# Optimization experiments

Hardware: AMD Instinct MI355X
Metric: run time of the kernel (lower is better)

The kernel has to match this reference:

```python
import jax, jax.numpy as jnp
import numpy as np

E = 8        # moe_num_experts
TOPK = 2     # moe_topk
H = 1024     # hidden_size
I = 1024     # intermediate_size
ISH = I * 2  # shared experts intermediate (intermediate_size * moe_num_shared_experts)
B, S = 2, 1024


def setup_inputs() -> dict:
    key = jax.random.key(0)
    ks = jax.random.split(key, 7)
    s = 0.02
    return {
        "hidden_states": jax.random.normal(ks[0], (B, S, H), jnp.float32),
        "w_router": jax.random.normal(ks[1], (H, E), jnp.float32) * s,
        "fc1_w": jax.random.normal(ks[2], (E, H, 2 * I), jnp.float32) * s,
        "fc2_w": jax.random.normal(ks[3], (E, I, H), jnp.float32) * s,
        "gate_w": jax.random.normal(ks[4], (H, ISH), jnp.float32) * s,
        "up_w": jax.random.normal(ks[5], (H, ISH), jnp.float32) * s,
        "down_w": jax.random.normal(ks[6], (ISH, H), jnp.float32) * s,
    }


def reference(hidden_states, w_router, fc1_w, fc2_w, gate_w, up_w, down_w):
    orig_shape = hidden_states.shape
    x = hidden_states.reshape(-1, orig_shape[-1])  # [N, H]

    # --- router: top-k + softmax over the top-k logits ---
    logits = x @ w_router                               # [N, E]
    top_logits, top_idx = jax.lax.top_k(logits, TOPK)   # [N, K]
    scores = jax.nn.softmax(top_logits, axis=-1)        # [N, K]

    # --- permute tokens so same-expert tokens are contiguous ---
    flat_idx = top_idx.reshape(-1)                      # [N*K]
    sorted_idx = jnp.argsort(flat_idx)                  # [N*K]
    permuted = x[sorted_idx // TOPK]                    # [N*K, H]
    eid = flat_idx[sorted_idx]                          # expert id per permuted slot

    # --- grouped expert SwiGLU MLP (masked per-expert GEMMs; masked rows
    #     contribute exactly zero since silu(0)*0 = 0 and 0 @ W = 0) ---
    out_perm = jnp.zeros((permuted.shape[0], orig_shape[-1]), x.dtype)
    for e in range(E):
        m = (eid == e).astype(x.dtype)[:, None]         # [N*K, 1]
        h1 = (permuted * m) @ fc1_w[e]                  # [N*K, 2I]
        proj, gate = jnp.split(h1, 2, axis=-1)
        out_perm = out_perm + (jax.nn.silu(proj) * gate) @ fc2_w[e]

    # --- unpermute and combine with router scores ---
    unperm = jnp.zeros_like(out_perm).at[sorted_idx].set(out_perm)  # [N*K, H]
    moe_out = (unperm.reshape(-1, TOPK, orig_shape[-1]) * scores[:, :, None]).sum(axis=1)
    moe_out = moe_out.reshape(orig_shape)

    # --- shared experts (LlamaMLP, SwiGLU) ---
    shared = (jax.nn.silu(hidden_states @ gate_w) * (hidden_states @ up_w)) @ down_w
    return moe_out + shared
```

## Files before the change

### kernel.cpp

```cpp
#include <hip/hip_runtime.h>
#include <cstdint>


#define E_ 8
#define H_ 1024
#define I_ 1024
#define ISH_ 2048
#define NTOK 2048

typedef unsigned short u16;
using bf16x8 = __attribute__((ext_vector_type(8))) __bf16;
using f32x4  = __attribute__((ext_vector_type(4))) float;

__device__ __forceinline__ u16 f2bf(float f) {
  union { float f; unsigned u; } v; v.f = f;
  unsigned r = v.u + 0x7fffu + ((v.u >> 16) & 1u);
  return (u16)(r >> 16);
}
__device__ __forceinline__ float bf2f(u16 u) {
  union { unsigned u; float f; } v; v.u = ((unsigned)u) << 16; return v.f;
}
__device__ __forceinline__ unsigned pk2(float lo, float hi) {
  return ((unsigned)f2bf(hi) << 16) | (unsigned)f2bf(lo);
}

typedef __attribute__((address_space(1))) const void glb_v;
typedef __attribute__((address_space(3))) void lds_v;
__device__ __forceinline__ void gl16(const void* g, void* l) {
  __builtin_amdgcn_global_load_lds((glb_v*)g, (lds_v*)l, 16, 0, 0);
}

__device__ __forceinline__ void router_body(const float* __restrict__ x,
                                            const float* __restrict__ wr,
                                            float* __restrict__ scores,
                                            int* __restrict__ cnt,
                                            int* __restrict__ list, int tk) {
  int lane = threadIdx.x & 63;
  const float* xr = x + (size_t)tk * H_;
  float acc[E_];
#pragma unroll
  for (int e = 0; e < E_; ++e) acc[e] = 0.f;
  int h0 = lane * 16;
#pragma unroll 4
  for (int i = 0; i < 16; ++i) {
    float xv = xr[h0 + i];
    const float* w = wr + (size_t)(h0 + i) * E_;
#pragma unroll
    for (int e = 0; e < E_; ++e) acc[e] = fmaf(xv, w[e], acc[e]);
  }
#pragma unroll
  for (int off = 32; off > 0; off >>= 1) {
#pragma unroll
    for (int e = 0; e < E_; ++e) acc[e] += __shfl_xor(acc[e], off, 64);
  }
  if (lane == 0) {
    int e0 = 0; float m0 = acc[0];
#pragma unroll
    for (int e = 1; e < E_; ++e) if (acc[e] > m0) { m0 = acc[e]; e0 = e; }
    int e1 = -1; float m1 = -1e30f;
#pragma unroll
    for (int e = 0; e < E_; ++e) if (e != e0 && acc[e] > m1) { m1 = acc[e]; e1 = e; }
    float s0 = 1.f / (1.f + __expf(m1 - m0));
    scores[tk * 2 + 0] = s0;
    scores[tk * 2 + 1] = 1.f - s0;
    int p0 = atomicAdd(&cnt[e0], 1); list[e0 * NTOK + p0] = tk * 2;
    int p1 = atomicAdd(&cnt[e1], 1); list[e1 * NTOK + p1] = tk * 2 + 1;
  }
}

__device__ __forceinline__ void wtrans(const float* __restrict__ src,
                                       u16* __restrict__ dst, int K, int N,
                                       int k0, int n0, void* smem) {
  unsigned* lt = (unsigned*)smem;
  int t = threadIdx.x;
  int c = t & 31, kb = t >> 5;
  const float* sp = src + (size_t)(k0 + kb * 8) * N + n0 + (c << 2);
  float v[8][4];
#pragma unroll
  for (int j2 = 0; j2 < 8; ++j2) {
    float4 f = *(const float4*)(sp + (size_t)j2 * N);
    v[j2][0] = f.x; v[j2][1] = f.y; v[j2][2] = f.z; v[j2][3] = f.w;
  }
#pragma unroll
  for (int j = 0; j < 4; ++j) {
    int nl = (c << 2) + j;
    uint4 o = make_uint4(pk2(v[0][j], v[1][j]), pk2(v[2][j], v[3][j]),
                         pk2(v[4][j], v[5][j]), pk2(v[6][j], v[7][j]));
    *(uint4*)&lt[nl * 32 + ((kb ^ (c & 7)) << 2)] = o;
  }
  __syncthreads();
#pragma unroll
  for (int it = 0; it < 4; ++it) {
    int lin = it * 256 + t;
    int nl = lin >> 3, kq = lin & 7;
    uint4 o = *(const uint4*)&lt[nl * 32 + ((kq ^ ((nl >> 2) & 7)) << 2)];
    *(uint4*)(dst + (size_t)(n0 + nl) * K + k0 + kq * 8) = o;
  }
}


__global__ __launch_bounds__(256) void prep_k(
    const float* __restrict__ x, const float* __restrict__ wr,
    float* __restrict__ scores, int* __restrict__ cnt, int* __restrict__ list,
    u16* __restrict__ xb,
    const float* __restrict__ fc1, const float* __restrict__ gw,
    const float* __restrict__ uw,
    u16* __restrict__ fc1T, u16* __restrict__ gwT, u16* __restrict__ uwT) {
  __shared__ __align__(16) char psm[16384];
  int bid = blockIdx.x, t = threadIdx.x;
  if (bid < 512) {
    router_body(x, wr, scores, cnt, list, bid * 4 + (t >> 6));
    return;
  }
  if (bid < 1024) {
    const float4* srcx = (const float4*)x;
    ushort4* dstx = (ushort4*)xb;
    int base = (bid - 512) * 1024 + t;
#pragma unroll
    for (int it = 0; it < 4; ++it) {
      float4 v = srcx[base + it * 256];
      ushort4 o;
      o.x = f2bf(v.x); o.y = f2bf(v.y); o.z = f2bf(v.z); o.w = f2bf(v.w);
      dstx[base + it * 256] = o;
    }
    return;
  }
  if (bid < 3072) {
    int b = bid - 1024;
    int e = b >> 8, q = b & 255;
    wtrans(fc1 + ((size_t)e << 21), fc1T + ((size_t)e << 21), 1024, 2048,
           (q & 15) * 64, (q >> 4) * 128, psm);
  } else if (bid < 3328) {
    int q = bid - 3072;
    wtrans(gw, gwT, 1024, 2048, (q & 15) * 64, (q >> 4) * 128, psm);
  } else {
    int q = bid - 3328;
    wtrans(uw, uwT, 1024, 2048, (q & 15) * 64, (q >> 4) * 128, psm);
  }
}

__global__ __launch_bounds__(256, 2) void swiglu_f_k(
    const u16* __restrict__ xb, const int* __restrict__ cnt,
    const int* __restrict__ list, const u16* __restrict__ fc1T,
    const u16* __restrict__ gwT, const u16* __restrict__ uwT,
    u16* __restrict__ act, u16* __restrict__ tmp,
    const float* __restrict__ fc2, const float* __restrict__ dw,
    u16* __restrict__ fc2T, u16* __restrict__ dwT) {
  __shared__ __align__(16) char smem[24576];
  if (blockIdx.x & 1) {
    int r = blockIdx.x >> 1;
    if (r < 1024) {
      int e = r >> 7, q = r & 127;
      wtrans(fc2 + ((size_t)e << 20), fc2T + ((size_t)e << 20), 1024, 1024,
             (q & 15) * 64, (q >> 4) * 128, smem);
    } else {
      int q = r - 1024;
      wtrans(dw, dwT, 2048, 1024, (q & 31) * 64, (q >> 5) * 128, smem);
    }
    return;
  }
  u16 (*As)[32]  = (u16(*)[32])smem;
  u16 (*B1s)[32] = (u16(*)[32])(smem + 8192);
  u16 (*B2s)[32] = (u16(*)[32])(smem + 16384);

  int bid = blockIdx.x >> 1;
  int m0, n0, Me, obase = 0, ldo;
  const u16 *B1, *B2;
  const int* rowmap = nullptr;
  u16* Out;
  if (bid < 256) {
    int mb = bid >> 4, nb = bid & 15;
    m0 = mb * 128; n0 = nb * 128; Me = NTOK;
    B1 = gwT + (size_t)n0 * 1024; B2 = uwT + (size_t)n0 * 1024;
    Out = tmp; ldo = ISH_;
  } else {
    int b2 = bid - 256; int e = b2 >> 7, r = b2 & 127, mb = r >> 3, nb = r & 7;
    Me = cnt[e]; m0 = mb * 128;
    if (m0 >= Me) return;
    n0 = nb * 128;
    rowmap = list + e * NTOK;
    const u16* fe = fc1T + ((size_t)e << 21);
    B1 = fe + (size_t)n0 * 1024;
    B2 = fe + (size_t)(1024 + n0) * 1024;
    int off = 0;
    for (int q = 0; q < e; ++q) off += cnt[q];
    obase = off;
    Out = act; ldo = I_;
  }
  int t = threadIdx.x, wid = t >> 6, lane = t & 63;
  int wm = wid & 1, wn = wid >> 1, lr = lane & 15, lkg = lane >> 4;
  int cq = lane & 3, crw = lane >> 2;

  const u16 *arow[2], *b1row[2], *b2row[2];
#pragma unroll
  for (int i = 0; i < 2; ++i) {
    int c = wid * 2 + i;
    int rl = m0 + c * 16 + crw;
    int rc = rl < Me ? rl : (Me - 1);
    int tok = rowmap ? (rowmap[rc] >> 1) : rc;
    arow[i] = xb + (size_t)tok * 1024 + cq * 8;
    int rb = c * 16 + crw;
    b1row[i] = B1 + (size_t)rb * 1024 + cq * 8;
    b2row[i] = B2 + (size_t)rb * 1024 + cq * 8;
  }

  f32x4 aP[4][4] = {}, aG[4][4] = {};
  for (int k0 = 0; k0 < 1024; k0 += 32) {
#pragma unroll
    for (int i = 0; i < 2; ++i) {
      int c = wid * 2 + i;
      gl16(arow[i] + k0, (u16*)As + c * 512);
      gl16(b1row[i] + k0, (u16*)B1s + c * 512);
      gl16(b2row[i] + k0, (u16*)B2s + c * 512);
    }
    __syncthreads();
    bf16x8 af[4];
#pragma unroll
    for (int f = 0; f < 4; ++f)
      af[f] = *reinterpret_cast<const bf16x8*>(&As[wm * 64 + f * 16 + lr][lkg * 8]);
#pragma unroll
    for (int fn = 0; fn < 4; ++fn) {
      bf16x8 b1 = *reinterpret_cast<const bf16x8*>(&B1s[wn * 64 + fn * 16 + lr][lkg * 8]);
      bf16x8 b2 = *reinterpret_cast<const bf16x8*>(&B2s[wn * 64 + fn * 16 + lr][lkg * 8]);
#pragma unroll
      for (int fm = 0; fm < 4; ++fm) {
        aP[fm][fn] = __builtin_amdgcn_mfma_f32_16x16x32_bf16(af[fm], b1, aP[fm][fn], 0, 0, 0);
        aG[fm][fn] = __builtin_amdgcn_mfma_f32_16x16x32_bf16(af[fm], b2, aG[fm][fn], 0, 0, 0);
      }
    }
    __syncthreads();
  }
#pragma unroll
  for (int fm = 0; fm < 4; ++fm)
#pragma unroll
    for (int fn = 0; fn < 4; ++fn)
#pragma unroll
      for (int j = 0; j < 4; ++j) {
        int row = m0 + wm * 64 + fm * 16 + lkg * 4 + j;
        if (row < Me) {
          float p = aP[fm][fn][j], g = aG[fm][fn][j];
          float s = p / (1.f + __expf(-p)) * g;
          Out[(size_t)(obase + row) * ldo + n0 + wn * 64 + fn * 16 + lr] = f2bf(s);
        }
      }
}

template <int MODE>
__global__ __launch_bounds__(256, 2) void gemm_f_k(
    const u16* __restrict__ A, const u16* __restrict__ Bg,
    const int* __restrict__ cnt, const int* __restrict__ list,
    const float* __restrict__ scores, u16* __restrict__ outb,
    const u16* __restrict__ outb_r, float* __restrict__ out) {
  constexpr int BNx = MODE == 0 ? 128 : 64;
  constexpr int FN = BNx / 32;
  constexpr int KK = MODE == 0 ? 1024 : 2048;
  constexpr int BCH = BNx / 64;
  __shared__ u16 As[128][32];
  __shared__ u16 Bs[BNx][32];
  int bid = blockIdx.x;
  int e = 0, m0, n0, Me, ks = 0;
  const u16 *Ab, *Bb;
  if (MODE == 0) {
    e = bid >> 7; int r = bid & 127, mb = r >> 3, nb = r & 7;
    Me = cnt[e]; m0 = mb * 128;
    if (m0 >= Me) return;
    n0 = nb * 128;
    int off = 0;
    for (int q = 0; q < e; ++q) off += cnt[q];
    Ab = A + (size_t)off * KK;
    Bb = Bg + ((size_t)e << 20) + (size_t)n0 * KK;
  } else {
    ks = bid >> 8; int r = bid & 255;
    int mb = r >> 4, nb = r & 15;
    m0 = mb * 128; n0 = nb * 64; Me = NTOK;
    Ab = A + ks * 1024;
    Bb = Bg + (size_t)n0 * KK + ks * 1024;
  }
  int t = threadIdx.x, wid = t >> 6, lane = t & 63;
  int wm = wid & 1, wn = wid >> 1, lr = lane & 15, lkg = lane >> 4;
  int cq = lane & 3, crw = lane >> 2;

  const u16* arow[2];
#pragma unroll
  for (int i = 0; i < 2; ++i) {
    int c = wid * 2 + i;
    int rl = m0 + c * 16 + crw;
    int rc = rl < Me ? rl : (Me - 1);
    arow[i] = Ab + (size_t)rc * KK + cq * 8;
  }
  const u16* brow[BCH];
#pragma unroll
  for (int i = 0; i < BCH; ++i) {
    int c = wid * BCH + i;
    brow[i] = Bb + (size_t)(c * 16 + crw) * KK + cq * 8;
  }

  f32x4 acc[4][FN] = {};
  for (int k0 = 0; k0 < 1024; k0 += 32) {
#pragma unroll
    for (int i = 0; i < 2; ++i) gl16(arow[i] + k0, (u16*)As + (wid * 2 + i) * 512);
#pragma unroll
    for (int i = 0; i < BCH; ++i) gl16(brow[i] + k0, (u16*)Bs + (wid * BCH + i) * 512);
    __syncthreads();
    bf16x8 af[4];
#pragma unroll
    for (int f = 0; f < 4; ++f)
      af[f] = *reinterpret_cast<const bf16x8*>(&As[wm * 64 + f * 16 + lr][lkg * 8]);
#pragma unroll
    for (int fn = 0; fn < FN; ++fn) {
      bf16x8 bb = *reinterpret_cast<const bf16x8*>(&Bs[wn * (BNx / 2) + fn * 16 + lr][lkg * 8]);
#pragma unroll
      for (int fm = 0; fm < 4; ++fm)
        acc[fm][fn] = __builtin_amdgcn_mfma_f32_16x16x32_bf16(af[fm], bb, acc[fm][fn], 0, 0, 0);
    }
    __syncthreads();
  }
#pragma unroll
  for (int fm = 0; fm < 4; ++fm)
#pragma unroll
    for (int fn = 0; fn < FN; ++fn)
#pragma unroll
      for (int j = 0; j < 4; ++j) {
        int row = m0 + wm * 64 + fm * 16 + lkg * 4 + j;
        if (row < Me) {
          float v = acc[fm][fn][j];
          int c = n0 + wn * (BNx / 2) + fn * 16 + lr;
          if (MODE == 0) {
            int slot = list[e * NTOK + row];
            outb[(size_t)slot * H_ + c] = f2bf(v * scores[slot]);
          } else {
            if (ks == 0)
              v += bf2f(outb_r[(size_t)(2 * row) * H_ + c]) +
                   bf2f(outb_r[(size_t)(2 * row + 1) * H_ + c]);
            atomicAdd(&out[(size_t)row * H_ + c], v);
          }
        }
      }
}

#define BM 128
#define BN 64
#define BK 32
#define PK (BK + 8)

__global__ void router_k(const float* __restrict__ x, const float* __restrict__ wr,
                         float* __restrict__ scores, int* __restrict__ cnt,
                         int* __restrict__ list) {
  int wid = threadIdx.x >> 6;
  int tk = blockIdx.x * 4 + wid;
  if (tk >= NTOK) return;
  router_body(x, wr, scores, cnt, list, tk);
}

__global__ void offs_k(const int* __restrict__ cnt, int* __restrict__ offs) {
  if (threadIdx.x == 0 && blockIdx.x == 0) {
    int s = 0;
    for (int e = 0; e < E_; ++e) { offs[e] = s; s += cnt[e]; }
  }
}

__global__ void cvt_k(const float* __restrict__ x, u16* __restrict__ xb, int n4) {
  int i = blockIdx.x * blockDim.x + threadIdx.x;
  if (i >= n4) return;
  float4 v = reinterpret_cast<const float4*>(x)[i];
  ushort4 o;
  o.x = f2bf(v.x); o.y = f2bf(v.y); o.z = f2bf(v.z); o.w = f2bf(v.w);
  reinterpret_cast<ushort4*>(xb)[i] = o;
}

template <int EXPERT>
__global__ __launch_bounds__(256) void swiglu_gemm_k(
    const u16* __restrict__ A, int lda,
    const int* __restrict__ list, const int* __restrict__ cnt, const int* __restrict__ offs,
    const float* __restrict__ B1g, const float* __restrict__ B2g, int ldb, long long bstride,
    u16* __restrict__ Out, int ldo, int K) {
  __shared__ u16 As[BM][PK];
  __shared__ u16 Bs[2][BN][PK];
  int e = EXPERT ? blockIdx.z : 0;
  int Me = EXPERT ? cnt[e] : NTOK;
  int m0 = blockIdx.y * BM;
  if (m0 >= Me) return;
  int n0 = blockIdx.x * BN;
  const int* rowmap = EXPERT ? (list + e * NTOK) : nullptr;
  const float* B1 = B1g + (EXPERT ? (long long)e * bstride : 0);
  const float* B2 = B2g + (EXPERT ? (long long)e * bstride : 0);
  int t = threadIdx.x, wid = t >> 6, lane = t & 63;
  int wm = wid & 1, wn = wid >> 1, lr = lane & 15, lkg = lane >> 4;
  f32x4 accP[4][2] = {}, accG[4][2] = {};
  for (int k0 = 0; k0 < K; k0 += BK) {
#pragma unroll
    for (int it = 0; it < 2; ++it) {
      int idx = it * 256 + t, r = idx >> 2, q = idx & 3, row = m0 + r;
      uint4 v = make_uint4(0u, 0u, 0u, 0u);
      if (row < Me) {
        int rg = EXPERT ? (rowmap[row] >> 1) : row;
        v = *reinterpret_cast<const uint4*>(A + (size_t)rg * lda + k0 + q * 8);
      }
      *reinterpret_cast<uint4*>(&As[r][q * 8]) = v;
    }
#pragma unroll
    for (int b = 0; b < 2; ++b) {
      const float* Bp = b ? B2 : B1;
#pragma unroll
      for (int it = 0; it < 2; ++it) {
        int idx = (it * 256 + t) * 4, kr = idx >> 6, c = idx & 63;
        float4 f = *reinterpret_cast<const float4*>(Bp + (size_t)(k0 + kr) * ldb + n0 + c);
        Bs[b][c + 0][kr] = f2bf(f.x); Bs[b][c + 1][kr] = f2bf(f.y);
        Bs[b][c + 2][kr] = f2bf(f.z); Bs[b][c + 3][kr] = f2bf(f.w);
      }
    }
    __syncthreads();
    bf16x8 af[4];
#pragma unroll
    for (int fm = 0; fm < 4; ++fm)
      af[fm] = *reinterpret_cast<const bf16x8*>(&As[wm * 64 + fm * 16 + lr][lkg * 8]);
#pragma unroll
    for (int fn = 0; fn < 2; ++fn) {
      bf16x8 bp = *reinterpret_cast<const bf16x8*>(&Bs[0][wn * 32 + fn * 16 + lr][lkg * 8]);
      bf16x8 bg = *reinterpret_cast<const bf16x8*>(&Bs[1][wn * 32 + fn * 16 + lr][lkg * 8]);
#pragma unroll
      for (int fm = 0; fm < 4; ++fm) {
        accP[fm][fn] = __builtin_amdgcn_mfma_f32_16x16x32_bf16(af[fm], bp, accP[fm][fn], 0, 0, 0);
        accG[fm][fn] = __builtin_amdgcn_mfma_f32_16x16x32_bf16(af[fm], bg, accG[fm][fn], 0, 0, 0);
      }
    }
    __syncthreads();
  }
#pragma unroll
  for (int fm = 0; fm < 4; ++fm)
#pragma unroll
    for (int fn = 0; fn < 2; ++fn)
#pragma unroll
      for (int j = 0; j < 4; ++j) {
        int grow = wm * 64 + fm * 16 + lkg * 4 + j, gcol = wn * 32 + fn * 16 + lr;
        int row = m0 + grow;
        if (row < Me) {
          float p = accP[fm][fn][j], g = accG[fm][fn][j];
          float s = p / (1.f + __expf(-p)) * g;
          int orow = EXPERT ? (offs[e] + row) : row;
          Out[(size_t)orow * ldo + n0 + gcol] = f2bf(s);
        }
      }
}

template <int EXPERT>
__global__ __launch_bounds__(256) void out_gemm_k(
    const u16* __restrict__ A, int lda,
    const int* __restrict__ cnt, const int* __restrict__ offs,
    const int* __restrict__ list, const float* __restrict__ scores,
    const float* __restrict__ Bg, int ldb, long long bstride,
    float* __restrict__ Out, const float* __restrict__ outbuf, int K) {
  __shared__ u16 As[BM][PK];
  __shared__ u16 Bs[BN][PK];
  int e = EXPERT ? blockIdx.z : 0;
  int Me = EXPERT ? cnt[e] : NTOK;
  int m0 = blockIdx.y * BM;
  if (m0 >= Me) return;
  int n0 = blockIdx.x * BN;
  const float* B = Bg + (EXPERT ? (long long)e * bstride : 0);
  int aoff = EXPERT ? offs[e] : 0;
  int t = threadIdx.x, wid = t >> 6, lane = t & 63;
  int wm = wid & 1, wn = wid >> 1, lr = lane & 15, lkg = lane >> 4;
  f32x4 acc[4][2] = {};
  for (int k0 = 0; k0 < K; k0 += BK) {
#pragma unroll
    for (int it = 0; it < 2; ++it) {
      int idx = it * 256 + t, r = idx >> 2, q = idx & 3, row = m0 + r;
      uint4 v = make_uint4(0u, 0u, 0u, 0u);
      if (row < Me)
        v = *reinterpret_cast<const uint4*>(A + (size_t)(aoff + row) * lda + k0 + q * 8);
      *reinterpret_cast<uint4*>(&As[r][q * 8]) = v;
    }
#pragma unroll
    for (int it = 0; it < 2; ++it) {
      int idx = (it * 256 + t) * 4, kr = idx >> 6, c = idx & 63;
      float4 f = *reinterpret_cast<const float4*>(B + (size_t)(k0 + kr) * ldb + n0 + c);
      Bs[c + 0][kr] = f2bf(f.x); Bs[c + 1][kr] = f2bf(f.y);
      Bs[c + 2][kr] = f2bf(f.z); Bs[c + 3][kr] = f2bf(f.w);
    }
    __syncthreads();
    bf16x8 af[4];
#pragma unroll
    for (int fm = 0; fm < 4; ++fm)
      af[fm] = *reinterpret_cast<const bf16x8*>(&As[wm * 64 + fm * 16 + lr][lkg * 8]);
#pragma unroll
    for (int fn = 0; fn < 2; ++fn) {
      bf16x8 bb = *reinterpret_cast<const bf16x8*>(&Bs[wn * 32 + fn * 16 + lr][lkg * 8]);
#pragma unroll
      for (int fm = 0; fm < 4; ++fm)
        acc[fm][fn] = __builtin_amdgcn_mfma_f32_16x16x32_bf16(af[fm], bb, acc[fm][fn], 0, 0, 0);
    }
    __syncthreads();
  }
#pragma unroll
  for (int fm = 0; fm < 4; ++fm)
#pragma unroll
    for (int fn = 0; fn < 2; ++fn)
#pragma unroll
      for (int j = 0; j < 4; ++j) {
        int grow = wm * 64 + fm * 16 + lkg * 4 + j, gcol = wn * 32 + fn * 16 + lr;
        int row = m0 + grow;
        if (row < Me) {
          float v = acc[fm][fn][j];
          int c = n0 + gcol;
          if (EXPERT) {
            int slot = list[e * NTOK + row];
            Out[(size_t)slot * H_ + c] = v * scores[slot];
          } else {
            Out[(size_t)row * H_ + c] =
                v + outbuf[(size_t)(2 * row) * H_ + c] + outbuf[(size_t)(2 * row + 1) * H_ + c];
          }
        }
      }
}

extern "C" void kernel_launch(void* const* d_in, const int* in_sizes, int n_in,
                              void* d_out, int out_size, void* d_ws, size_t ws_size,
                              hipStream_t stream) {
  const float* x   = (const float*)d_in[0];
  const float* wr  = (const float*)d_in[1];
  const float* fc1 = (const float*)d_in[2];
  const float* fc2 = (const float*)d_in[3];
  const float* gw  = (const float*)d_in[4];
  const float* uw  = (const float*)d_in[5];
  const float* dw  = (const float*)d_in[6];
  float* out = (float*)d_out;
  char* ws = (char*)d_ws;

  const size_t NEED_FAST = 131072ull + (88ull << 20);
  if (ws_size >= NEED_FAST) {
    float* scores = (float*)ws;
    int* cnt  = (int*)(ws + 16384);
    int* list = (int*)(ws + 16512);
    u16* xb   = (u16*)(ws + 131072);
    u16* act  = (u16*)(ws + 131072 + (4ll << 20));
    u16* tmp  = (u16*)(ws + 131072 + (12ll << 20));
    u16* outb = (u16*)(ws + 131072 + (20ll << 20));
    u16* fc1T = (u16*)(ws + 131072 + (28ll << 20));
    u16* fc2T = (u16*)(ws + 131072 + (60ll << 20));
    u16* gwT  = (u16*)(ws + 131072 + (76ll << 20));
    u16* uwT  = (u16*)(ws + 131072 + (80ll << 20));
    u16* dwT  = (u16*)(ws + 131072 + (84ll << 20));

    hipMemsetAsync(cnt, 0, 128, stream);
    hipMemsetAsync(out, 0, (size_t)NTOK * H_ * sizeof(float), stream);
    prep_k<<<3584, 256, 0, stream>>>(x, wr, scores, cnt, list, xb,
                                     fc1, gw, uw, fc1T, gwT, uwT);
    swiglu_f_k<<<2560, 256, 0, stream>>>(xb, cnt, list, fc1T, gwT, uwT, act, tmp,
                                         fc2, dw, fc2T, dwT);
    gemm_f_k<0><<<1024, 256, 0, stream>>>(act, fc2T, cnt, list, scores, outb, nullptr, nullptr);
    gemm_f_k<1><<<512, 256, 0, stream>>>(tmp, dwT, nullptr, nullptr, nullptr, nullptr, outb, out);
  } else {
    float* scores = (float*)(ws);
    int*   cnt    = (int*)(ws + (16 << 10));
    int*   offs   = (int*)(ws + (16 << 10) + 128);
    int*   list   = (int*)(ws + (16 << 10) + 256);
    u16*   xb     = (u16*)(ws + (96 << 10));
    u16*   act    = (u16*)(ws + (96 << 10) + (4ll << 20));
    u16*   tmp    = (u16*)(ws + (96 << 10) + (12ll << 20));
    float* outbuf = (float*)(ws + (96 << 10) + (20ll << 20));

    hipMemsetAsync(cnt, 0, E_ * sizeof(int), stream);
    router_k<<<NTOK / 4, 256, 0, stream>>>(x, wr, scores, cnt, list);
    offs_k<<<1, 64, 0, stream>>>(cnt, offs);
    cvt_k<<<(NTOK * H_ / 4 + 255) / 256, 256, 0, stream>>>(x, xb, NTOK * H_ / 4);
    swiglu_gemm_k<1><<<dim3(I_ / BN, NTOK / BM, E_), 256, 0, stream>>>(
        xb, H_, list, cnt, offs, fc1, fc1 + I_, 2 * I_, (long long)H_ * 2 * I_, act, I_, H_);
    out_gemm_k<1><<<dim3(H_ / BN, NTOK / BM, E_), 256, 0, stream>>>(
        act, I_, cnt, offs, list, scores, fc2, H_, (long long)I_ * H_, outbuf, nullptr, I_);
    swiglu_gemm_k<0><<<dim3(ISH_ / BN, NTOK / BM, 1), 256, 0, stream>>>(
        xb, H_, nullptr, nullptr, nullptr, gw, uw, ISH_, 0, tmp, ISH_, H_);
    out_gemm_k<0><<<dim3(H_ / BN, NTOK / BM, 1), 256, 0, stream>>>(
        tmp, ISH_, nullptr, nullptr, nullptr, nullptr, dw, H_, 0, out, outbuf, ISH_);
  }
  (void)in_sizes; (void)n_in; (void)out_size;
}
```

Measured before the change: 274.4 us.

## Double-buffer LDS in GEMMs, merge output GEMMs, move weight transposes to prep

Adds double-buffered LDS staging to the SwiGLU and output GEMMs, so the loads for the next K tile are issued before computing on the current one. The fc2 and down weight transposes move out of the SwiGLU kernel and into the prep kernel. The routed-expert and shared down-projection GEMMs merge into one launch that atomically adds straight into the output, which removes the bf16 outb intermediate and one kernel launch. In exchange, LDS per block doubles, which may lower occupancy, and there are more float atomics on the output.

```diff
diff --git a/kernel.cpp b/kernel.cpp
--- a/kernel.cpp
+++ b/kernel.cpp
@@ -103,9 +103,11 @@
     const float* __restrict__ x, const float* __restrict__ wr,
     float* __restrict__ scores, int* __restrict__ cnt, int* __restrict__ list,
     u16* __restrict__ xb,
-    const float* __restrict__ fc1, const float* __restrict__ gw,
-    const float* __restrict__ uw,
-    u16* __restrict__ fc1T, u16* __restrict__ gwT, u16* __restrict__ uwT) {
+    const float* __restrict__ fc1, const float* __restrict__ fc2,
+    const float* __restrict__ gw, const float* __restrict__ uw,
+    const float* __restrict__ dw,
+    u16* __restrict__ fc1T, u16* __restrict__ fc2T, u16* __restrict__ gwT,
+    u16* __restrict__ uwT, u16* __restrict__ dwT) {
   __shared__ __align__(16) char psm[16384];
   int bid = blockIdx.x, t = threadIdx.x;
   if (bid < 512) {
@@ -133,9 +135,17 @@
   } else if (bid < 3328) {
     int q = bid - 3072;
     wtrans(gw, gwT, 1024, 2048, (q & 15) * 64, (q >> 4) * 128, psm);
-  } else {
+  } else if (bid < 3584) {
     int q = bid - 3328;
     wtrans(uw, uwT, 1024, 2048, (q & 15) * 64, (q >> 4) * 128, psm);
+  } else if (bid < 4608) {
+    int b = bid - 3584;
+    int e = b >> 7, q = b & 127;
+    wtrans(fc2 + ((size_t)e << 20), fc2T + ((size_t)e << 20), 1024, 1024,
+           (q & 15) * 64, (q >> 4) * 128, psm);
+  } else {
+    int q = bid - 4608;
+    wtrans(dw, dwT, 2048, 1024, (q & 31) * 64, (q >> 5) * 128, psm);
   }
 }
 
@@ -143,27 +153,12 @@
     const u16* __restrict__ xb, const int* __restrict__ cnt,
     const int* __restrict__ list, const u16* __restrict__ fc1T,
     const u16* __restrict__ gwT, const u16* __restrict__ uwT,
-    u16* __restrict__ act, u16* __restrict__ tmp,
-    const float* __restrict__ fc2, const float* __restrict__ dw,
-    u16* __restrict__ fc2T, u16* __restrict__ dwT) {
-  __shared__ __align__(16) char smem[24576];
-  if (blockIdx.x & 1) {
-    int r = blockIdx.x >> 1;
-    if (r < 1024) {
-      int e = r >> 7, q = r & 127;
-      wtrans(fc2 + ((size_t)e << 20), fc2T + ((size_t)e << 20), 1024, 1024,
-             (q & 15) * 64, (q >> 4) * 128, smem);
-    } else {
-      int q = r - 1024;
-      wtrans(dw, dwT, 2048, 1024, (q & 31) * 64, (q >> 5) * 128, smem);
-    }
-    return;
-  }
-  u16 (*As)[32]  = (u16(*)[32])smem;
-  u16 (*B1s)[32] = (u16(*)[32])(smem + 8192);
-  u16 (*B2s)[32] = (u16(*)[32])(smem + 16384);
-
-  int bid = blockIdx.x >> 1;
+    u16* __restrict__ act, u16* __restrict__ tmp) {
+  __shared__ __align__(16) u16 As[2][128][32];
+  __shared__ __align__(16) u16 B1s[2][128][32];
+  __shared__ __align__(16) u16 B2s[2][128][32];
+
+  int bid = blockIdx.x;
   int m0, n0, Me, obase = 0, ldo;
   const u16 *B1, *B2;
   const int* rowmap = nullptr;
@@ -204,32 +199,45 @@
     b2row[i] = B2 + (size_t)rb * 1024 + cq * 8;
   }
 
-  f32x4 aP[4][4] = {}, aG[4][4] = {};
-  for (int k0 = 0; k0 < 1024; k0 += 32) {
+  auto stage = [&](int cb, int kk) {
 #pragma unroll
     for (int i = 0; i < 2; ++i) {
       int c = wid * 2 + i;
-      gl16(arow[i] + k0, (u16*)As + c * 512);
-      gl16(b1row[i] + k0, (u16*)B1s + c * 512);
-      gl16(b2row[i] + k0, (u16*)B2s + c * 512);
-    }
-    __syncthreads();
+      gl16(arow[i] + kk, (u16*)As + cb * 4096 + c * 512);
+      gl16(b1row[i] + kk, (u16*)B1s + cb * 4096 + c * 512);
+      gl16(b2row[i] + kk, (u16*)B2s + cb * 4096 + c * 512);
+    }
+  };
+
+  f32x4 aP[4][4] = {}, aG[4][4] = {};
+  auto compute = [&](int cb) {
     bf16x8 af[4];
 #pragma unroll
     for (int f = 0; f < 4; ++f)
-      af[f] = *reinterpret_cast<const bf16x8*>(&As[wm * 64 + f * 16 + lr][lkg * 8]);
+      af[f] = *(const bf16x8*)((u16*)As + cb * 4096 + (wm * 64 + f * 16 + lr) * 32 + lkg * 8);
 #pragma unroll
     for (int fn = 0; fn < 4; ++fn) {
-      bf16x8 b1 = *reinterpret_cast<const bf16x8*>(&B1s[wn * 64 + fn * 16 + lr][lkg * 8]);
-      bf16x8 b2 = *reinterpret_cast<const bf16x8*>(&B2s[wn * 64 + fn * 16 + lr][lkg * 8]);
+      bf16x8 b1 = *(const bf16x8*)((u16*)B1s + cb * 4096 + (wn * 64 + fn * 16 + lr) * 32 + lkg * 8);
+      bf16x8 b2 = *(const bf16x8*)((u16*)B2s + cb * 4096 + (wn * 64 + fn * 16 + lr) * 32 + lkg * 8);
 #pragma unroll
       for (int fm = 0; fm < 4; ++fm) {
         aP[fm][fn] = __builtin_amdgcn_mfma_f32_16x16x32_bf16(af[fm], b1, aP[fm][fn], 0, 0, 0);
         aG[fm][fn] = __builtin_amdgcn_mfma_f32_16x16x32_bf16(af[fm], b2, aG[fm][fn], 0, 0, 0);
       }
     }
+  };
+
+  stage(0, 0);
+  __syncthreads();
+  int cur = 0;
+  for (int k0 = 32; k0 < 1024; k0 += 32) {
+    stage(cur ^ 1, k0);
+    compute(cur);
     __syncthreads();
-  }
+    cur ^= 1;
+  }
+  compute(cur);
+
 #pragma unroll
   for (int fm = 0; fm < 4; ++fm)
 #pragma unroll
@@ -246,36 +254,17 @@
 }
 
 template <int MODE>
-__global__ __launch_bounds__(256, 2) void gemm_f_k(
-    const u16* __restrict__ A, const u16* __restrict__ Bg,
-    const int* __restrict__ cnt, const int* __restrict__ list,
-    const float* __restrict__ scores, u16* __restrict__ outb,
-    const u16* __restrict__ outb_r, float* __restrict__ out) {
-  constexpr int BNx = MODE == 0 ? 128 : 64;
+__device__ __forceinline__ void out_body(
+    const u16* __restrict__ Ab, const u16* __restrict__ Bb, int Me, int m0,
+    int n0, const int* __restrict__ listE, const float* __restrict__ scores,
+    float* __restrict__ out, char* smem) {
+  constexpr int BNx = MODE ? 64 : 128;
   constexpr int FN = BNx / 32;
-  constexpr int KK = MODE == 0 ? 1024 : 2048;
+  constexpr int KROW = MODE ? 2048 : 1024;
   constexpr int BCH = BNx / 64;
-  __shared__ u16 As[128][32];
-  __shared__ u16 Bs[BNx][32];
-  int bid = blockIdx.x;
-  int e = 0, m0, n0, Me, ks = 0;
-  const u16 *Ab, *Bb;
-  if (MODE == 0) {
-    e = bid >> 7; int r = bid & 127, mb = r >> 3, nb = r & 7;
-    Me = cnt[e]; m0 = mb * 128;
-    if (m0 >= Me) return;
-    n0 = nb * 128;
-    int off = 0;
-    for (int q = 0; q < e; ++q) off += cnt[q];
-    Ab = A + (size_t)off * KK;
-    Bb = Bg + ((size_t)e << 20) + (size_t)n0 * KK;
-  } else {
-    ks = bid >> 8; int r = bid & 255;
-    int mb = r >> 4, nb = r & 15;
-    m0 = mb * 128; n0 = nb * 64; Me = NTOK;
-    Ab = A + ks * 1024;
-    Bb = Bg + (size_t)n0 * KK + ks * 1024;
-  }
+  u16* As = (u16*)smem;
+  u16* Bs = (u16*)(smem + 16384);
+
   int t = threadIdx.x, wid = t >> 6, lane = t & 63;
   int wm = wid & 1, wn = wid >> 1, lr = lane & 15, lkg = lane >> 4;
   int cq = lane & 3, crw = lane >> 2;
@@ -286,35 +275,51 @@
     int c = wid * 2 + i;
     int rl = m0 + c * 16 + crw;
     int rc = rl < Me ? rl : (Me - 1);
-    arow[i] = Ab + (size_t)rc * KK + cq * 8;
+    arow[i] = Ab + (size_t)rc * KROW + cq * 8;
   }
   const u16* brow[BCH];
 #pragma unroll
   for (int i = 0; i < BCH; ++i) {
     int c = wid * BCH + i;
-    brow[i] = Bb + (size_t)(c * 16 + crw) * KK + cq * 8;
-  }
+    brow[i] = Bb + (size_t)(c * 16 + crw) * KROW + cq * 8;
+  }
+
+  auto stage = [&](int cb, int kk) {
+#pragma unroll
+    for (int i = 0; i < 2; ++i)
+      gl16(arow[i] + kk, As + cb * 4096 + (wid * 2 + i) * 512);
+#pragma unroll
+    for (int i = 0; i < BCH; ++i)
+      gl16(brow[i] + kk, Bs + cb * (BNx * 32) + (wid * BCH + i) * 512);
+  };
 
   f32x4 acc[4][FN] = {};
-  for (int k0 = 0; k0 < 1024; k0 += 32) {
-#pragma unroll
-    for (int i = 0; i < 2; ++i) gl16(arow[i] + k0, (u16*)As + (wid * 2 + i) * 512);
-#pragma unroll
-    for (int i = 0; i < BCH; ++i) gl16(brow[i] + k0, (u16*)Bs + (wid * BCH + i) * 512);
-    __syncthreads();
+  auto compute = [&](int cb) {
     bf16x8 af[4];
 #pragma unroll
     for (int f = 0; f < 4; ++f)
-      af[f] = *reinterpret_cast<const bf16x8*>(&As[wm * 64 + f * 16 + lr][lkg * 8]);
+      af[f] = *(const bf16x8*)(As + cb * 4096 + (wm * 64 + f * 16 + lr) * 32 + lkg * 8);
 #pragma unroll
     for (int fn = 0; fn < FN; ++fn) {
-      bf16x8 bb = *reinterpret_cast<const bf16x8*>(&Bs[wn * (BNx / 2) + fn * 16 + lr][lkg * 8]);
+      bf16x8 bb = *(const bf16x8*)(Bs + cb * (BNx * 32) +
+                                   (wn * (BNx / 2) + fn * 16 + lr) * 32 + lkg * 8);
 #pragma unroll
       for (int fm = 0; fm < 4; ++fm)
         acc[fm][fn] = __builtin_amdgcn_mfma_f32_16x16x32_bf16(af[fm], bb, acc[fm][fn], 0, 0, 0);
     }
+  };
+
+  stage(0, 0);
+  __syncthreads();
+  int cur = 0;
+  for (int k0 = 32; k0 < 1024; k0 += 32) {
+    stage(cur ^ 1, k0);
+    compute(cur);
     __syncthreads();
-  }
+    cur ^= 1;
+  }
+  compute(cur);
+
 #pragma unroll
   for (int fm = 0; fm < 4; ++fm)
 #pragma unroll
@@ -326,16 +331,37 @@
           float v = acc[fm][fn][j];
           int c = n0 + wn * (BNx / 2) + fn * 16 + lr;
           if (MODE == 0) {
-            int slot = list[e * NTOK + row];
-            outb[(size_t)slot * H_ + c] = f2bf(v * scores[slot]);
+            int slot = listE[row];
+            atomicAdd(&out[(size_t)(slot >> 1) * H_ + c], v * scores[slot]);
           } else {
-            if (ks == 0)
-              v += bf2f(outb_r[(size_t)(2 * row) * H_ + c]) +
-                   bf2f(outb_r[(size_t)(2 * row + 1) * H_ + c]);
             atomicAdd(&out[(size_t)row * H_ + c], v);
           }
         }
       }
+}
+
+__global__ __launch_bounds__(256, 2) void out_f_k(
+    const u16* __restrict__ act, const u16* __restrict__ fc2T,
+    const u16* __restrict__ tmp, const u16* __restrict__ dwT,
+    const int* __restrict__ cnt, const int* __restrict__ list,
+    const float* __restrict__ scores, float* __restrict__ out) {
+  __shared__ __align__(16) char smem[32768];
+  int bid = blockIdx.x;
+  if (bid < 1024) {
+    int e = bid >> 7, r = bid & 127, mb = r >> 3, nb = r & 7;
+    int Me = cnt[e], m0 = mb * 128;
+    if (m0 >= Me) return;
+    int off = 0;
+    for (int q = 0; q < e; ++q) off += cnt[q];
+    out_body<0>(act + (size_t)off * 1024,
+                fc2T + ((size_t)e << 20) + (size_t)(nb * 128) * 1024,
+                Me, m0, nb * 128, list + e * NTOK, scores, out, smem);
+  } else {
+    int r = bid - 1024, ks = r >> 8, rr = r & 255, mb = rr >> 4, nb = rr & 15;
+    out_body<1>(tmp + ks * 1024,
+                dwT + (size_t)(nb * 64) * 2048 + ks * 1024,
+                NTOK, mb * 128, nb * 64, nullptr, nullptr, out, smem);
+  }
 }
 
 #define BM 128
@@ -535,7 +561,6 @@
     u16* xb   = (u16*)(ws + 131072);
     u16* act  = (u16*)(ws + 131072 + (4ll << 20));
     u16* tmp  = (u16*)(ws + 131072 + (12ll << 20));
-    u16* outb = (u16*)(ws + 131072 + (20ll << 20));
     u16* fc1T = (u16*)(ws + 131072 + (28ll << 20));
     u16* fc2T = (u16*)(ws + 131072 + (60ll << 20));
     u16* gwT  = (u16*)(ws + 131072 + (76ll << 20));
@@ -544,12 +569,11 @@
 
     hipMemsetAsync(cnt, 0, 128, stream);
     hipMemsetAsync(out, 0, (size_t)NTOK * H_ * sizeof(float), stream);
-    prep_k<<<3584, 256, 0, stream>>>(x, wr, scores, cnt, list, xb,
-                                     fc1, gw, uw, fc1T, gwT, uwT);
-    swiglu_f_k<<<2560, 256, 0, stream>>>(xb, cnt, list, fc1T, gwT, uwT, act, tmp,
-                                         fc2, dw, fc2T, dwT);
-    gemm_f_k<0><<<1024, 256, 0, stream>>>(act, fc2T, cnt, list, scores, outb, nullptr, nullptr);
-    gemm_f_k<1><<<512, 256, 0, stream>>>(tmp, dwT, nullptr, nullptr, nullptr, nullptr, outb, out);
+    prep_k<<<4864, 256, 0, stream>>>(x, wr, scores, cnt, list, xb,
+                                     fc1, fc2, gw, uw, dw,
+                                     fc1T, fc2T, gwT, uwT, dwT);
+    swiglu_f_k<<<1280, 256, 0, stream>>>(xb, cnt, list, fc1T, gwT, uwT, act, tmp);
+    out_f_k<<<1536, 256, 0, stream>>>(act, fc2T, tmp, dwT, cnt, list, scores, out);
   } else {
     float* scores = (float*)(ws);
     int*   cnt    = (int*)(ws + (16 << 10));
```

After: 254.4 us. 1.08x faster.
